# Performance work log

Hardware: AMD Instinct MI355X
Metric: run time of the kernel (lower is better)

The kernel has to match this reference:

```python
import jax, jax.numpy as jnp
import numpy as np

B = 32768
N_TABLES = 26
N_ROWS = 200000
D = 64
N_DENSE = 13
NUM_PAIRS = (N_TABLES + 1) * N_TABLES // 2  # 351, pairs j < i over 27 vectors


def setup_inputs() -> dict:
    key = jax.random.key(0)
    ks = jax.random.split(key, 16)
    def lin(kw, kb, m, n):
        W = jax.random.normal(kw, (m, n), jnp.float32) * np.sqrt(2.0 / (m + n))
        b = jax.random.normal(kb, (m,), jnp.float32) * np.sqrt(1.0 / m)
        return W, b
    bw0, bb0 = lin(ks[0], ks[1], 512, N_DENSE)
    bw1, bb1 = lin(ks[2], ks[3], 256, 512)
    bw2, bb2 = lin(ks[4], ks[5], D, 256)
    tw0, tb0 = lin(ks[6], ks[7], 512, D + NUM_PAIRS)
    tw1, tb1 = lin(ks[8], ks[9], 256, 512)
    tw2, tb2 = lin(ks[10], ks[11], 1, 256)
    bound = np.sqrt(1.0 / N_ROWS)
    emb_tables = jax.random.uniform(ks[12], (N_TABLES, N_ROWS, D), jnp.float32,
                                    minval=-bound, maxval=bound)
    dense_x = jax.random.uniform(ks[13], (B, N_DENSE), jnp.float32)
    indices = jax.random.randint(ks[14], (N_TABLES, B), 0, N_ROWS, jnp.int64)
    return {"dense_x": dense_x, "indices": indices, "emb_tables": emb_tables,
            "bw0": bw0, "bb0": bb0, "bw1": bw1, "bb1": bb1, "bw2": bw2, "bb2": bb2,
            "tw0": tw0, "tb0": tb0, "tw1": tw1, "tb1": tb1, "tw2": tw2, "tb2": tb2}


def reference(dense_x, indices, emb_tables,
              bw0, bb0, bw1, bb1, bw2, bb2,
              tw0, tb0, tw1, tb1, tw2, tb2):
    # bottom MLP (all ReLU, sigmoid_bot = -1)
    h = jax.nn.relu(dense_x @ bw0.T + bb0)
    h = jax.nn.relu(h @ bw1.T + bb1)
    x_bot = jax.nn.relu(h @ bw2.T + bb2)          # [B, D]

    # multi-table EmbeddingBag(sum) with single-index bags -> plain gather
    embs = jax.vmap(lambda tbl, idx: tbl[idx])(emb_tables, indices)  # [26, B, D]

    # dot interaction over 27 feature vectors
    T = jnp.concatenate([x_bot[None], embs], axis=0).transpose(1, 0, 2)  # [B, 27, D]
    Z = jnp.einsum('bnd,bmd->bnm', T, T)                                 # [B, 27, 27]
    li, lj = jnp.tril_indices(N_TABLES + 1, k=-1)  # pairs with j < i (no self)
    Zflat = Z[:, li, lj]                           # [B, 351]
    R = jnp.concatenate([x_bot, Zflat], axis=1)    # [B, 415]

    # top MLP: ReLU, ReLU, Sigmoid (sigmoid_top = 2)
    h = jax.nn.relu(R @ tw0.T + tb0)
    h = jax.nn.relu(h @ tw1.T + tb1)
    p = jax.nn.sigmoid(h @ tw2.T + tb2)            # [B, 1]
    return p
```

## Files before the change

kernel.cpp:

```cpp
#include <hip/hip_runtime.h>
#include <cstddef>
#include <cstdint>

#define B_SZ    32768
#define NTAB    26
#define NROWS   200000

typedef __attribute__((ext_vector_type(8))) short short8v;
typedef __attribute__((ext_vector_type(4))) float f32x4;
typedef __attribute__((ext_vector_type(16))) float f32x16;

__device__ __forceinline__ ushort f2bf(float f) {
    uint32_t u = __builtin_bit_cast(uint32_t, f);
    u += 0x7FFFu + ((u >> 16) & 1u);
    return (ushort)(u >> 16);
}
__device__ __forceinline__ void stage16(const ushort* g, ushort* l) {
    __builtin_amdgcn_global_load_lds(
        (const __attribute__((address_space(1))) unsigned int*)g,
        (__attribute__((address_space(3))) unsigned int*)l, 16, 0, 0);
}

__global__ __launch_bounds__(256) void conv_all_k(
    const float* __restrict__ dense_x, const float* __restrict__ bw0,
    const float* __restrict__ tw0, const float* __restrict__ bw1,
    const float* __restrict__ bw2, const float* __restrict__ tw1,
    ushort* __restrict__ dense_pad, ushort* __restrict__ bw0p,
    ushort* __restrict__ tw0p, ushort* __restrict__ bw1c,
    ushort* __restrict__ bw2c, ushort* __restrict__ tw1c)
{
    const int gid = blockIdx.x * 256 + threadIdx.x;
    if (gid < 1048576) {
        int r = gid >> 5, k = gid & 31;
        dense_pad[gid] = (k < 13) ? f2bf(dense_x[r * 13 + k]) : (ushort)0;
    } else if (gid < 1064960) {
        int i = gid - 1048576; int r = i >> 5, k = i & 31;
        bw0p[i] = (k < 13) ? f2bf(bw0[r * 13 + k]) : (ushort)0;
    } else if (gid < 1277952) {
        int i = gid - 1064960; int r = i / 416, k = i - r * 416;
        tw0p[i] = (k < 415) ? f2bf(tw0[r * 415 + k]) : (ushort)0;
    } else if (gid < 1409024) {
        int i = gid - 1277952; bw1c[i] = f2bf(bw1[i]);
    } else if (gid < 1425408) {
        int i = gid - 1409024; bw2c[i] = f2bf(bw2[i]);
    } else if (gid < 1556480) {
        int i = gid - 1425408; tw1c[i] = f2bf(tw1[i]);
    }
}

__global__ __launch_bounds__(256, 2) void fused_k(
    const ushort* __restrict__ dense_pad, const ushort* __restrict__ bw0p,
    const float* __restrict__ bb0, const ushort* __restrict__ bw1c,
    const float* __restrict__ bb1, const ushort* __restrict__ bw2c,
    const float* __restrict__ bb2,
    const float* __restrict__ emb, const int* __restrict__ indices,
    const ushort* __restrict__ tw0p, const float* __restrict__ tb0,
    const ushort* __restrict__ tw1c, const float* __restrict__ tb1,
    const float* __restrict__ tw2, const float* __restrict__ tb2,
    float* __restrict__ out)
{
    __shared__ __align__(16) ushort R1[32 * 512];
    __shared__ __align__(16) ushort Wst[2][256 * 32];
    __shared__ __align__(16) ushort R3[32 * 256];
    ushort* const Wf = &Wst[0][0];
    const int t = threadIdx.x;
    const int lane = t & 63, w = t >> 6;
    const int fr = lane & 15, j16 = lane >> 4;
    const int bBase = blockIdx.x * 32;

    int ir0, ir1, ir2, ir3;
    ir0 = indices[(size_t)(t >> 5) * B_SZ + bBase + (t & 31)];
    ir1 = indices[(size_t)((256 + t) >> 5) * B_SZ + bBase + ((256 + t) & 31)];
    ir2 = indices[(size_t)((512 + t) >> 5) * B_SZ + bBase + ((512 + t) & 31)];
    ir3 = (t < 64) ? indices[(size_t)((768 + t) >> 5) * B_SZ + bBase + ((768 + t) & 31)] : 0;

    if (t < 128) {
        const int r = t >> 2, u = t & 3, us = u ^ ((r >> 1) & 3);
        stage16(dense_pad + (size_t)(bBase + r) * 32 + us * 8, &R3[t * 8]);
    }
#pragma unroll
    for (int i = 0; i < 4; ++i) {
        const int idx = i * 256 + t;
        const int r = idx >> 2, u = idx & 3, us = u ^ ((r >> 1) & 3);
        stage16(bw0p + (size_t)r * 32 + us * 8, &Wst[0][idx * 8]);
        stage16(bw0p + (size_t)(256 + r) * 32 + us * 8, &Wst[1][idx * 8]);
    }
    __syncthreads();

    f32x4 acc0[2][2][4] = {};
    {
        short8v a[2];
#pragma unroll
        for (int m = 0; m < 2; ++m) {
            const int r = m * 16 + fr;
            a[m] = *(const short8v*)&R3[r * 32 + (j16 ^ ((r >> 1) & 3)) * 8];
        }
#pragma unroll
        for (int hh = 0; hh < 2; ++hh) {
            short8v b[4];
#pragma unroll
            for (int n = 0; n < 4; ++n) {
                const int lr = w * 64 + n * 16 + fr;
                b[n] = *(const short8v*)&Wst[hh][lr * 32 + (j16 ^ ((lr >> 1) & 3)) * 8];
            }
            __builtin_amdgcn_s_setprio(1);
#pragma unroll
            for (int m = 0; m < 2; ++m)
#pragma unroll
                for (int n = 0; n < 4; ++n)
                    acc0[hh][m][n] = __builtin_amdgcn_mfma_f32_16x16x32_bf16(b[n], a[m], acc0[hh][m][n], 0, 0, 0);
            __builtin_amdgcn_s_setprio(0);
        }
    }
    __syncthreads();

#pragma unroll
    for (int i = 0; i < 4; ++i) {
        const int idx = i * 256 + t;
        const int r = idx >> 2, u = idx & 3, us = u ^ ((r >> 1) & 3);
        stage16(bw1c + (size_t)r * 512 + us * 8, &Wst[0][idx * 8]);
        stage16(bw1c + (size_t)r * 512 + 32 + us * 8, &Wst[1][idx * 8]);
    }
#pragma unroll
    for (int hh = 0; hh < 2; ++hh)
#pragma unroll
    for (int n = 0; n < 4; ++n) {
        const int ch = hh * 256 + w * 64 + n * 16 + j16 * 4;
        const float4 bv = *(const float4*)&bb0[ch];
#pragma unroll
        for (int m = 0; m < 2; ++m) {
            const int s = m * 16 + fr;
            ushort4 o;
            o.x = f2bf(fmaxf(acc0[hh][m][n][0] + bv.x, 0.f));
            o.y = f2bf(fmaxf(acc0[hh][m][n][1] + bv.y, 0.f));
            o.z = f2bf(fmaxf(acc0[hh][m][n][2] + bv.z, 0.f));
            o.w = f2bf(fmaxf(acc0[hh][m][n][3] + bv.w, 0.f));
            const int u = ch >> 3, su = u ^ (s & 7);
            *(ushort4*)&R1[s * 512 + su * 8 + (ch & 7)] = o;
        }
    }
    __syncthreads();

    f32x4 acc1[2][4] = {};
    for (int i8 = 0; i8 < 8; ++i8) {
#pragma unroll
        for (int half = 0; half < 2; ++half) {
            const int kt = i8 * 64 + half * 32;
            short8v a[2], b[4];
#pragma unroll
            for (int m = 0; m < 2; ++m) {
                const int s = m * 16 + fr;
                const int u = (kt >> 3) + j16, su = u ^ (s & 7);
                a[m] = *(const short8v*)&R1[s * 512 + su * 8];
            }
#pragma unroll
            for (int n = 0; n < 4; ++n) {
                const int lr = w * 64 + n * 16 + fr;
                b[n] = *(const short8v*)&Wst[half][lr * 32 + (j16 ^ ((lr >> 1) & 3)) * 8];
            }
            __builtin_amdgcn_s_setprio(1);
#pragma unroll
            for (int m = 0; m < 2; ++m)
#pragma unroll
                for (int n = 0; n < 4; ++n)
                    acc1[m][n] = __builtin_amdgcn_mfma_f32_16x16x32_bf16(b[n], a[m], acc1[m][n], 0, 0, 0);
            __builtin_amdgcn_s_setprio(0);
        }
        __syncthreads();
        if (i8 < 7) {
            const int kt2 = (i8 + 1) * 64;
#pragma unroll
            for (int i = 0; i < 4; ++i) {
                const int idx = i * 256 + t;
                const int r = idx >> 2, u = idx & 3, us = u ^ ((r >> 1) & 3);
                stage16(bw1c + (size_t)r * 512 + kt2 + us * 8, &Wst[0][idx * 8]);
                stage16(bw1c + (size_t)r * 512 + kt2 + 32 + us * 8, &Wst[1][idx * 8]);
            }
            __syncthreads();
        }
    }
#pragma unroll
    for (int i = 0; i < 8; ++i) {
        const int idx = i * 256 + t;
        const int st = idx >> 8, within = idx & 255;
        const int r = within >> 2, u = within & 3, us = u ^ ((r >> 1) & 3);
        stage16(bw2c + (size_t)r * 256 + st * 32 + us * 8, &Wf[idx * 8]);
    }
#pragma unroll
    for (int n = 0; n < 4; ++n) {
        const int ch = w * 64 + n * 16 + j16 * 4;
        const float4 bv = *(const float4*)&bb1[ch];
#pragma unroll
        for (int m = 0; m < 2; ++m) {
            const int s = m * 16 + fr;
            ushort4 o;
            o.x = f2bf(fmaxf(acc1[m][n][0] + bv.x, 0.f));
            o.y = f2bf(fmaxf(acc1[m][n][1] + bv.y, 0.f));
            o.z = f2bf(fmaxf(acc1[m][n][2] + bv.z, 0.f));
            o.w = f2bf(fmaxf(acc1[m][n][3] + bv.w, 0.f));
            const int u = ch >> 3, su = u ^ (s & 7);
            *(ushort4*)&R3[s * 256 + su * 8 + (ch & 7)] = o;
        }
    }
    __syncthreads();

    f32x4 acc2[2] = {};
    for (int kt = 0; kt < 256; kt += 32) {
        short8v a[2], b;
#pragma unroll
        for (int m = 0; m < 2; ++m) {
            const int s = m * 16 + fr;
            const int u = (kt >> 3) + j16, su = u ^ (s & 7);
            a[m] = *(const short8v*)&R3[s * 256 + su * 8];
        }
        {
            const int lr = w * 16 + fr;
            b = *(const short8v*)&Wf[(kt >> 5) * 2048 + lr * 32 + (j16 ^ ((lr >> 1) & 3)) * 8];
        }
#pragma unroll
        for (int m = 0; m < 2; ++m)
            acc2[m] = __builtin_amdgcn_mfma_f32_16x16x32_bf16(b, a[m], acc2[m], 0, 0, 0);
    }
    __syncthreads();

#pragma unroll
    for (int i = 0; i < 4; ++i) {
        const int idx = i * 256 + t;
        const int r = idx >> 2, u = idx & 3, us = u ^ ((r >> 1) & 3);
        stage16(tw0p + (size_t)r * 416 + us * 8, &Wst[0][idx * 8]);
        stage16(tw0p + (size_t)(256 + r) * 416 + us * 8, &Wst[1][idx * 8]);
    }
    {
        const int ch = w * 16 + j16 * 4;
        const float4 bv = *(const float4*)&bb2[ch];
#pragma unroll
        for (int m = 0; m < 2; ++m) {
            const int s = m * 16 + fr;
            ushort4 o;
            o.x = f2bf(fmaxf(acc2[m][0] + bv.x, 0.f));
            o.y = f2bf(fmaxf(acc2[m][1] + bv.y, 0.f));
            o.z = f2bf(fmaxf(acc2[m][2] + bv.z, 0.f));
            o.w = f2bf(fmaxf(acc2[m][3] + bv.w, 0.f));
            *(ushort4*)&R1[s * 424 + ch] = o;
        }
    }
    if (t < 32) R1[t * 424 + 415] = 0;
    {
        int* sc = (int*)R3;
        sc[t] = ir0; sc[256 + t] = ir1; sc[512 + t] = ir2;
        if (t < 64) sc[768 + t] = ir3;
    }
    __syncthreads();

    {
        const int* sc = (const int*)R3;
        const int r32 = lane & 31, half = lane >> 5;
        const bool isEmb = (r32 >= 1) && (r32 <= 26);
        const size_t tblOfs = isEmb ? (size_t)(r32 - 1) * NROWS : 0;

#define LOADRAW(dst, s_) { \
        const int idxv = isEmb ? sc[(r32 - 1) * 32 + (s_)] : 0; \
        const float* rp = emb + (tblOfs + (size_t)idxv) * 64 + half * 8; \
        _Pragma("unroll") \
        for (int kq = 0; kq < 4; ++kq) { \
            dst[2 * kq]     = *(const f32x4*)&rp[kq * 16]; \
            dst[2 * kq + 1] = *(const f32x4*)&rp[kq * 16 + 4]; } }

#define COMPUTE(raw, s_) { \
        short8v tf[4]; \
        _Pragma("unroll") \
        for (int kq = 0; kq < 4; ++kq) { \
            short8v v; \
            v[0] = (short)f2bf(raw[2 * kq][0]);     v[1] = (short)f2bf(raw[2 * kq][1]); \
            v[2] = (short)f2bf(raw[2 * kq][2]);     v[3] = (short)f2bf(raw[2 * kq][3]); \
            v[4] = (short)f2bf(raw[2 * kq + 1][0]); v[5] = (short)f2bf(raw[2 * kq + 1][1]); \
            v[6] = (short)f2bf(raw[2 * kq + 1][2]); v[7] = (short)f2bf(raw[2 * kq + 1][3]); \
            if (r32 == 0) v = *(const short8v*)&R1[(s_) * 424 + kq * 16 + half * 8]; \
            else if (!isEmb) v = (short8v)0; \
            tf[kq] = v; } \
        f32x16 c = {}; \
        _Pragma("unroll") \
        for (int kq = 0; kq < 4; ++kq) \
            c = __builtin_amdgcn_mfma_f32_32x32x16_bf16(tf[kq], tf[kq], c, 0, 0, 0); \
        _Pragma("unroll") \
        for (int reg = 0; reg < 16; ++reg) { \
            const int r = (reg & 3) + 8 * (reg >> 2) + 4 * half; \
            if (r < 27 && r32 < r) \
                R1[(s_) * 424 + 64 + (r * (r - 1)) / 2 + r32] = f2bf(c[reg]); } }

        f32x4 rawA[8], rawB[8];
        LOADRAW(rawA, w);
#pragma unroll
        for (int p = 0; p < 4; ++p) {
            const int sA = p * 8 + w;
            const int sB = p * 8 + 4 + w;
            LOADRAW(rawB, sB);
            COMPUTE(rawA, sA);
            if (p < 3) LOADRAW(rawA, p * 8 + 8 + w);
            COMPUTE(rawB, sB);
        }
#undef LOADRAW
#undef COMPUTE
    }
    __syncthreads();

    f32x4 accA[2][2][4] = {};
    for (int kt_i = 0; kt_i < 13; ++kt_i) {
        const int kt = kt_i * 32;
        short8v a[2];
#pragma unroll
        for (int m = 0; m < 2; ++m) {
            const int s = m * 16 + fr;
            a[m] = *(const short8v*)&R1[s * 424 + ((kt >> 3) + j16) * 8];
        }
#pragma unroll
        for (int hh = 0; hh < 2; ++hh) {
            short8v b[4];
#pragma unroll
            for (int n = 0; n < 4; ++n) {
                const int lr = w * 64 + n * 16 + fr;
                b[n] = *(const short8v*)&Wst[hh][lr * 32 + (j16 ^ ((lr >> 1) & 3)) * 8];
            }
            __builtin_amdgcn_s_setprio(1);
#pragma unroll
            for (int m = 0; m < 2; ++m)
#pragma unroll
                for (int n = 0; n < 4; ++n)
                    accA[hh][m][n] = __builtin_amdgcn_mfma_f32_16x16x32_bf16(b[n], a[m], accA[hh][m][n], 0, 0, 0);
            __builtin_amdgcn_s_setprio(0);
        }
        __syncthreads();
        if (kt_i < 12) {
            const int kt2 = kt + 32;
#pragma unroll
            for (int i = 0; i < 4; ++i) {
                const int idx = i * 256 + t;
                const int r = idx >> 2, u = idx & 3, us = u ^ ((r >> 1) & 3);
                stage16(tw0p + (size_t)r * 416 + kt2 + us * 8, &Wst[0][idx * 8]);
                stage16(tw0p + (size_t)(256 + r) * 416 + kt2 + us * 8, &Wst[1][idx * 8]);
            }
            __syncthreads();
        }
    }
#pragma unroll
    for (int i = 0; i < 4; ++i) {
        const int idx = i * 256 + t;
        const int r = idx >> 2, u = idx & 3, us = u ^ ((r >> 1) & 3);
        stage16(tw1c + (size_t)r * 512 + us * 8, &Wst[0][idx * 8]);
        stage16(tw1c + (size_t)r * 512 + 32 + us * 8, &Wst[1][idx * 8]);
    }
#pragma unroll
    for (int hh = 0; hh < 2; ++hh)
#pragma unroll
    for (int n = 0; n < 4; ++n) {
        const int ch = hh * 256 + w * 64 + n * 16 + j16 * 4;
        const float4 bv = *(const float4*)&tb0[ch];
#pragma unroll
        for (int m = 0; m < 2; ++m) {
            const int s = m * 16 + fr;
            ushort4 o;
            o.x = f2bf(fmaxf(accA[hh][m][n][0] + bv.x, 0.f));
            o.y = f2bf(fmaxf(accA[hh][m][n][1] + bv.y, 0.f));
            o.z = f2bf(fmaxf(accA[hh][m][n][2] + bv.z, 0.f));
            o.w = f2bf(fmaxf(accA[hh][m][n][3] + bv.w, 0.f));
            const int u = ch >> 3, su = u ^ (s & 7);
            *(ushort4*)&R1[s * 512 + su * 8 + (ch & 7)] = o;
        }
    }
    __syncthreads();

    f32x4 accB[2][4] = {};
    for (int i8 = 0; i8 < 8; ++i8) {
#pragma unroll
        for (int half = 0; half < 2; ++half) {
            const int kt = i8 * 64 + half * 32;
            short8v a[2], b[4];
#pragma unroll
            for (int m = 0; m < 2; ++m) {
                const int s = m * 16 + fr;
                const int u = (kt >> 3) + j16, su = u ^ (s & 7);
                a[m] = *(const short8v*)&R1[s * 512 + su * 8];
            }
#pragma unroll
            for (int n = 0; n < 4; ++n) {
                const int lr = w * 64 + n * 16 + fr;
                b[n] = *(const short8v*)&Wst[half][lr * 32 + (j16 ^ ((lr >> 1) & 3)) * 8];
            }
            __builtin_amdgcn_s_setprio(1);
#pragma unroll
            for (int m = 0; m < 2; ++m)
#pragma unroll
                for (int n = 0; n < 4; ++n)
                    accB[m][n] = __builtin_amdgcn_mfma_f32_16x16x32_bf16(b[n], a[m], accB[m][n], 0, 0, 0);
            __builtin_amdgcn_s_setprio(0);
        }
        __syncthreads();
        if (i8 < 7) {
            const int kt2 = (i8 + 1) * 64;
#pragma unroll
            for (int i = 0; i < 4; ++i) {
                const int idx = i * 256 + t;
                const int r = idx >> 2, u = idx & 3, us = u ^ ((r >> 1) & 3);
                stage16(tw1c + (size_t)r * 512 + kt2 + us * 8, &Wst[0][idx * 8]);
                stage16(tw1c + (size_t)r * 512 + kt2 + 32 + us * 8, &Wst[1][idx * 8]);
            }
            __syncthreads();
        }
    }

    float* red = (float*)R3;
    float part[2] = {0.f, 0.f};
#pragma unroll
    for (int n = 0; n < 4; ++n) {
        const int ch = w * 64 + n * 16 + j16 * 4;
        const float4 bv = *(const float4*)&tb1[ch];
        const float4 wv = *(const float4*)&tw2[ch];
#pragma unroll
        for (int m = 0; m < 2; ++m) {
            part[m] += fmaxf(accB[m][n][0] + bv.x, 0.f) * wv.x
                     + fmaxf(accB[m][n][1] + bv.y, 0.f) * wv.y
                     + fmaxf(accB[m][n][2] + bv.z, 0.f) * wv.z
                     + fmaxf(accB[m][n][3] + bv.w, 0.f) * wv.w;
        }
    }
#pragma unroll
    for (int m = 0; m < 2; ++m) {
        float v = part[m];
        v += __shfl_xor(v, 16, 64);
        v += __shfl_xor(v, 32, 64);
        if (lane < 16) red[w * 32 + m * 16 + fr] = v;
    }
    __syncthreads();
    if (t < 32) {
        const float sm = red[t] + red[32 + t] + red[64 + t] + red[96 + t];
        out[bBase + t] = 1.f / (1.f + expf(-(sm + tb2[0])));
    }
}

extern "C" void kernel_launch(void* const* d_in, const int* in_sizes, int n_in,
                              void* d_out, int out_size, void* d_ws, size_t ws_size,
                              hipStream_t stream)
{
    (void)in_sizes; (void)n_in; (void)out_size; (void)ws_size;
    const float* dense_x = (const float*)d_in[0];
    const int*   indices = (const int*)d_in[1];
    const float* emb     = (const float*)d_in[2];
    const float* bw0 = (const float*)d_in[3];
    const float* bb0 = (const float*)d_in[4];
    const float* bw1 = (const float*)d_in[5];
    const float* bb1 = (const float*)d_in[6];
    const float* bw2 = (const float*)d_in[7];
    const float* bb2 = (const float*)d_in[8];
    const float* tw0 = (const float*)d_in[9];
    const float* tb0 = (const float*)d_in[10];
    const float* tw1 = (const float*)d_in[11];
    const float* tb1 = (const float*)d_in[12];
    const float* tw2 = (const float*)d_in[13];
    const float* tb2 = (const float*)d_in[14];
    float* out = (float*)d_out;

    ushort* ws16      = (ushort*)d_ws;
    ushort* dense_pad = ws16;
    ushort* bw0p      = dense_pad + (size_t)B_SZ * 32;
    ushort* tw0p      = bw0p + 512 * 32;
    ushort* bw1c      = tw0p + 512 * 416;
    ushort* bw2c      = bw1c + 256 * 512;
    ushort* tw1c      = bw2c + 64 * 256;

    conv_all_k<<<dim3(6080), dim3(256), 0, stream>>>(
        dense_x, bw0, tw0, bw1, bw2, tw1,
        dense_pad, bw0p, tw0p, bw1c, bw2c, tw1c);

    fused_k<<<dim3(B_SZ / 32), dim3(256), 0, stream>>>(
        dense_pad, bw0p, bb0, bw1c, bb1, bw2c, bb2,
        emb, indices, tw0p, tb0, tw1c, tb1, tw2, tb2, out);
}
```

Before: 108.7 us.

## Double-buffer weight stages with counted vmcnt waits across three MLP GEMMs

Restructures the weight-streaming loops of the 512x256 bottom layer and the two top-MLP GEMMs. Each 32-wide K slice now goes into alternating LDS buffers, with the load for slice st+2 issued while slice st+1 is consumed. The full __syncthreads after each load is replaced by a partial s_waitcnt vmcnt(4) plus a raw barrier, so the global-to-LDS copies overlap with MFMA work instead of stalling it. In exchange there are more barrier points, and correctness depends on the exact count of outstanding memory ops and on the prologue having issued the first two stages into the right buffers.

```diff
diff --git a/kernel.cpp b/kernel.cpp
--- a/kernel.cpp
+++ b/kernel.cpp
@@ -19,6 +19,18 @@
     __builtin_amdgcn_global_load_lds(
         (const __attribute__((address_space(1))) unsigned int*)g,
         (__attribute__((address_space(3))) unsigned int*)l, 16, 0, 0);
+}
+__device__ __forceinline__ void wait_stage_then_barrier(bool last) {
+    if (last) asm volatile("s_waitcnt vmcnt(0)" ::: "memory");
+    else      asm volatile("s_waitcnt vmcnt(4)" ::: "memory");
+    __builtin_amdgcn_sched_barrier(0);
+    __builtin_amdgcn_s_barrier();
+    __builtin_amdgcn_sched_barrier(0);
+}
+__device__ __forceinline__ void reads_done_barrier() {
+    __builtin_amdgcn_sched_barrier(0);
+    __builtin_amdgcn_s_barrier();
+    __builtin_amdgcn_sched_barrier(0);
 }
 
 __global__ __launch_bounds__(256) void conv_all_k(
@@ -142,41 +154,37 @@
     __syncthreads();
 
     f32x4 acc1[2][4] = {};
-    for (int i8 = 0; i8 < 8; ++i8) {
-#pragma unroll
-        for (int half = 0; half < 2; ++half) {
-            const int kt = i8 * 64 + half * 32;
-            short8v a[2], b[4];
-#pragma unroll
-            for (int m = 0; m < 2; ++m) {
-                const int s = m * 16 + fr;
-                const int u = (kt >> 3) + j16, su = u ^ (s & 7);
-                a[m] = *(const short8v*)&R1[s * 512 + su * 8];
-            }
-#pragma unroll
-            for (int n = 0; n < 4; ++n) {
-                const int lr = w * 64 + n * 16 + fr;
-                b[n] = *(const short8v*)&Wst[half][lr * 32 + (j16 ^ ((lr >> 1) & 3)) * 8];
-            }
-            __builtin_amdgcn_s_setprio(1);
-#pragma unroll
-            for (int m = 0; m < 2; ++m)
-#pragma unroll
-                for (int n = 0; n < 4; ++n)
-                    acc1[m][n] = __builtin_amdgcn_mfma_f32_16x16x32_bf16(b[n], a[m], acc1[m][n], 0, 0, 0);
-            __builtin_amdgcn_s_setprio(0);
-        }
-        __syncthreads();
-        if (i8 < 7) {
-            const int kt2 = (i8 + 1) * 64;
+    for (int st = 0; st < 16; ++st) {
+        wait_stage_then_barrier(st == 15);
+        const int kt = st * 32;
+        short8v a[2], b[4];
+#pragma unroll
+        for (int m = 0; m < 2; ++m) {
+            const int s = m * 16 + fr;
+            const int u = (kt >> 3) + j16, su = u ^ (s & 7);
+            a[m] = *(const short8v*)&R1[s * 512 + su * 8];
+        }
+#pragma unroll
+        for (int n = 0; n < 4; ++n) {
+            const int lr = w * 64 + n * 16 + fr;
+            b[n] = *(const short8v*)&Wst[st & 1][lr * 32 + (j16 ^ ((lr >> 1) & 3)) * 8];
+        }
+        __builtin_amdgcn_s_setprio(1);
+#pragma unroll
+        for (int m = 0; m < 2; ++m)
+#pragma unroll
+            for (int n = 0; n < 4; ++n)
+                acc1[m][n] = __builtin_amdgcn_mfma_f32_16x16x32_bf16(b[n], a[m], acc1[m][n], 0, 0, 0);
+        __builtin_amdgcn_s_setprio(0);
+        reads_done_barrier();
+        if (st + 2 < 16) {
+            const int kt2 = (st + 2) * 32;
 #pragma unroll
             for (int i = 0; i < 4; ++i) {
                 const int idx = i * 256 + t;
                 const int r = idx >> 2, u = idx & 3, us = u ^ ((r >> 1) & 3);
-                stage16(bw1c + (size_t)r * 512 + kt2 + us * 8, &Wst[0][idx * 8]);
-                stage16(bw1c + (size_t)r * 512 + kt2 + 32 + us * 8, &Wst[1][idx * 8]);
+                stage16(bw1c + (size_t)r * 512 + kt2 + us * 8, &Wst[st & 1][idx * 8]);
             }
-            __syncthreads();
         }
     }
 #pragma unroll
@@ -305,41 +313,37 @@
     __syncthreads();
 
     f32x4 accA[2][2][4] = {};
-    for (int kt_i = 0; kt_i < 13; ++kt_i) {
-        const int kt = kt_i * 32;
-        short8v a[2];
+    for (int st = 0; st < 26; ++st) {
+        wait_stage_then_barrier(st == 25);
+        const int kt = (st >> 1) * 32, hh = st & 1;
+        short8v a[2], b[4];
 #pragma unroll
         for (int m = 0; m < 2; ++m) {
             const int s = m * 16 + fr;
             a[m] = *(const short8v*)&R1[s * 424 + ((kt >> 3) + j16) * 8];
         }
 #pragma unroll
-        for (int hh = 0; hh < 2; ++hh) {
-            short8v b[4];
-#pragma unroll
-            for (int n = 0; n < 4; ++n) {
-                const int lr = w * 64 + n * 16 + fr;
-                b[n] = *(const short8v*)&Wst[hh][lr * 32 + (j16 ^ ((lr >> 1) & 3)) * 8];
-            }
-            __builtin_amdgcn_s_setprio(1);
-#pragma unroll
-            for (int m = 0; m < 2; ++m)
-#pragma unroll
-                for (int n = 0; n < 4; ++n)
-                    accA[hh][m][n] = __builtin_amdgcn_mfma_f32_16x16x32_bf16(b[n], a[m], accA[hh][m][n], 0, 0, 0);
-            __builtin_amdgcn_s_setprio(0);
-        }
-        __syncthreads();
-        if (kt_i < 12) {
-            const int kt2 = kt + 32;
+        for (int n = 0; n < 4; ++n) {
+            const int lr = w * 64 + n * 16 + fr;
+            b[n] = *(const short8v*)&Wst[st & 1][lr * 32 + (j16 ^ ((lr >> 1) & 3)) * 8];
+        }
+        __builtin_amdgcn_s_setprio(1);
+#pragma unroll
+        for (int m = 0; m < 2; ++m)
+#pragma unroll
+            for (int n = 0; n < 4; ++n)
+                accA[hh][m][n] = __builtin_amdgcn_mfma_f32_16x16x32_bf16(b[n], a[m], accA[hh][m][n], 0, 0, 0);
+        __builtin_amdgcn_s_setprio(0);
+        reads_done_barrier();
+        if (st + 2 < 26) {
+            const int st2 = st + 2;
+            const int kt2 = (st2 >> 1) * 32, hh2 = st2 & 1;
 #pragma unroll
             for (int i = 0; i < 4; ++i) {
                 const int idx = i * 256 + t;
                 const int r = idx >> 2, u = idx & 3, us = u ^ ((r >> 1) & 3);
-                stage16(tw0p + (size_t)r * 416 + kt2 + us * 8, &Wst[0][idx * 8]);
-                stage16(tw0p + (size_t)(256 + r) * 416 + kt2 + us * 8, &Wst[1][idx * 8]);
+                stage16(tw0p + (size_t)(hh2 * 256 + r) * 416 + kt2 + us * 8, &Wst[st & 1][idx * 8]);
             }
-            __syncthreads();
         }
     }
 #pragma unroll
@@ -370,41 +374,37 @@
     __syncthreads();
 
     f32x4 accB[2][4] = {};
-    for (int i8 = 0; i8 < 8; ++i8) {
-#pragma unroll
-        for (int half = 0; half < 2; ++half) {
-            const int kt = i8 * 64 + half * 32;
-            short8v a[2], b[4];
-#pragma unroll
-            for (int m = 0; m < 2; ++m) {
-                const int s = m * 16 + fr;
-                const int u = (kt >> 3) + j16, su = u ^ (s & 7);
-                a[m] = *(const short8v*)&R1[s * 512 + su * 8];
-            }
-#pragma unroll
-            for (int n = 0; n < 4; ++n) {
-                const int lr = w * 64 + n * 16 + fr;
-                b[n] = *(const short8v*)&Wst[half][lr * 32 + (j16 ^ ((lr >> 1) & 3)) * 8];
-            }
-            __builtin_amdgcn_s_setprio(1);
-#pragma unroll
-            for (int m = 0; m < 2; ++m)
-#pragma unroll
-                for (int n = 0; n < 4; ++n)
-                    accB[m][n] = __builtin_amdgcn_mfma_f32_16x16x32_bf16(b[n], a[m], accB[m][n], 0, 0, 0);
-            __builtin_amdgcn_s_setprio(0);
-        }
-        __syncthreads();
-        if (i8 < 7) {
-            const int kt2 = (i8 + 1) * 64;
+    for (int st = 0; st < 16; ++st) {
+        wait_stage_then_barrier(st == 15);
+        const int kt = st * 32;
+        short8v a[2], b[4];
+#pragma unroll
+        for (int m = 0; m < 2; ++m) {
+            const int s = m * 16 + fr;
+            const int u = (kt >> 3) + j16, su = u ^ (s & 7);
+            a[m] = *(const short8v*)&R1[s * 512 + su * 8];
+        }
+#pragma unroll
+        for (int n = 0; n < 4; ++n) {
+            const int lr = w * 64 + n * 16 + fr;
+            b[n] = *(const short8v*)&Wst[st & 1][lr * 32 + (j16 ^ ((lr >> 1) & 3)) * 8];
+        }
+        __builtin_amdgcn_s_setprio(1);
+#pragma unroll
+        for (int m = 0; m < 2; ++m)
+#pragma unroll
+            for (int n = 0; n < 4; ++n)
+                accB[m][n] = __builtin_amdgcn_mfma_f32_16x16x32_bf16(b[n], a[m], accB[m][n], 0, 0, 0);
+        __builtin_amdgcn_s_setprio(0);
+        reads_done_barrier();
+        if (st + 2 < 16) {
+            const int kt2 = (st + 2) * 32;
 #pragma unroll
             for (int i = 0; i < 4; ++i) {
                 const int idx = i * 256 + t;
                 const int r = idx >> 2, u = idx & 3, us = u ^ ((r >> 1) & 3);
-                stage16(tw1c + (size_t)r * 512 + kt2 + us * 8, &Wst[0][idx * 8]);
-                stage16(tw1c + (size_t)r * 512 + kt2 + 32 + us * 8, &Wst[1][idx * 8]);
+                stage16(tw1c + (size_t)r * 512 + kt2 + us * 8, &Wst[st & 1][idx * 8]);
             }
-            __syncthreads();
         }
     }
 
```

Measured after the change: 111.5 us. +2.5%, slower.
